# Kernel tuning notes

Hardware: AMD Instinct MI355X
Metric: run time of the kernel (lower is better)

## Reference

```python
import jax, jax.numpy as jnp
import numpy as np

B, T, D, HS = 4, 2048, 1024, 64


def setup_inputs() -> dict:
    key = jax.random.key(0)
    ks = jax.random.split(key, 8)
    s = 0.02
    return {
        "x": jax.random.normal(ks[0], (B, T, D), dtype=jnp.float32),
        "wq": jax.random.normal(ks[1], (D, HS), dtype=jnp.float32) * s,
        "bq": jax.random.normal(ks[2], (HS,), dtype=jnp.float32) * s,
        "wk": jax.random.normal(ks[3], (D, HS), dtype=jnp.float32) * s,
        "bk": jax.random.normal(ks[4], (HS,), dtype=jnp.float32) * s,
        "wv": jax.random.normal(ks[5], (D, HS), dtype=jnp.float32) * s,
        "bv": jax.random.normal(ks[6], (HS,), dtype=jnp.float32) * s,
        "rel_pos_embd": jax.random.normal(ks[7], (T, T, HS), dtype=jnp.float32) * s,
    }


def reference(x, wq, bq, wk, bk, wv, bv, rel_pos_embd):
    # x: [B,T,D]
    q = jnp.einsum("btd,dh->bth", x, wq) + bq  # [B,T,HS]
    k = jnp.einsum("btd,dh->bth", x, wk) + bk
    v = jnp.einsum("btd,dh->bth", x, wv) + bv
    hs = k.shape[-1]
    # faithful to torch: scores = QK^T / hs**(-0.5) == QK^T * sqrt(hs)
    scores = jnp.einsum("bth,bvh->btv", q, k) * jnp.sqrt(jnp.float32(hs))
    # relative-position bias (mask=False branch)
    rel = jnp.einsum("btc,tvc->btv", q, rel_pos_embd[:q.shape[1], :q.shape[1]])
    att = jax.nn.softmax(scores + rel, axis=-1)  # [B,T,T]
    return jnp.einsum("btv,bvh->bth", att, v)  # [B,T,HS]
```

## Files before the change

kernel.cpp:

```cpp
#include <hip/hip_runtime.h>

#define B_ 4
#define T_ 2048
#define D_ 1024
#define HS_ 64

typedef __attribute__((ext_vector_type(4))) float f32x4;
typedef __attribute__((ext_vector_type(8))) short bf16x8;
typedef __attribute__((ext_vector_type(4))) unsigned short u16x4;
typedef __attribute__((ext_vector_type(4))) unsigned int u32x4;

__device__ __forceinline__ unsigned short f2bf(float f) {
  unsigned int u = __float_as_uint(f);
  u += 0x7FFFu + ((u >> 16) & 1u);
  return (unsigned short)(u >> 16);
}

__global__ void kconv_kernel(const float* __restrict__ wq, const float* __restrict__ wk,
                             const float* __restrict__ wv,
                             unsigned short* __restrict__ wTh, unsigned short* __restrict__ wTl) {
  int gid = blockIdx.x * 256 + threadIdx.x;
  int n = gid >> 10, d = gid & 1023;
  float v;
  if (n < 64)        v = wq[d * 64 + n];
  else if (n < 128)  v = 8.0f * wk[d * 64 + (n - 64)];
  else               v = wv[d * 64 + (n - 128)];
  unsigned short h = f2bf(v);
  wTh[gid] = h;
  wTl[gid] = f2bf(v - __uint_as_float(((unsigned int)h) << 16));
}

__global__ __launch_bounds__(256) void kproj_kernel(
    const float* __restrict__ x, const unsigned short* __restrict__ wTh,
    const unsigned short* __restrict__ wTl,
    const float* __restrict__ bq, const float* __restrict__ bk, const float* __restrict__ bv,
    float* __restrict__ qw, float* __restrict__ k8w, unsigned short* __restrict__ vtw) {
  __shared__ unsigned short xh[32 * 32], xl[32 * 32];
  __shared__ unsigned short wh[192 * 32], wl[192 * 32];
  const int tid = threadIdx.x;
  const int m0 = blockIdx.x * 32;
  const int lane = tid & 63, wid = tid >> 6;
  const int mf = wid & 1, np = wid >> 1;
  const int r15 = lane & 15, u = lane >> 4;

  f32x4 xv;
  f32x4 wvh[3], wvl[3];
  auto issue = [&](int k0) {
    xv = *(const f32x4*)&x[(m0 + (tid >> 3)) * 1024 + k0 + (tid & 7) * 4];
#pragma unroll
    for (int i = 0; i < 3; ++i) {
      int c8 = i * 256 + tid;
      wvh[i] = *(const f32x4*)&wTh[(c8 >> 2) * 1024 + k0 + (c8 & 3) * 8];
      wvl[i] = *(const f32x4*)&wTl[(c8 >> 2) * 1024 + k0 + (c8 & 3) * 8];
    }
  };
  auto commit = [&]() {
    u16x4 hhv, llv;
#pragma unroll
    for (int c = 0; c < 4; ++c) {
      unsigned short h = f2bf(xv[c]);
      hhv[c] = h;
      llv[c] = f2bf(xv[c] - __uint_as_float(((unsigned int)h) << 16));
    }
    *(u16x4*)&xh[(tid >> 3) * 32 + (tid & 7) * 4] = hhv;
    *(u16x4*)&xl[(tid >> 3) * 32 + (tid & 7) * 4] = llv;
#pragma unroll
    for (int i = 0; i < 3; ++i) {
      int c8 = i * 256 + tid;
      *(f32x4*)&wh[c8 * 8] = wvh[i];
      *(f32x4*)&wl[c8 * 8] = wvl[i];
    }
  };

  f32x4 z = {0.f, 0.f, 0.f, 0.f};
  f32x4 acc[6] = {z, z, z, z, z, z};
  issue(0);
  for (int kt = 0; kt < 32; ++kt) {
    __syncthreads();
    commit();
    __syncthreads();
    if (kt + 1 < 32) issue((kt + 1) * 32);
    bf16x8 ah = *(const bf16x8*)&xh[(mf * 16 + r15) * 32 + u * 8];
    bf16x8 al = *(const bf16x8*)&xl[(mf * 16 + r15) * 32 + u * 8];
#pragma unroll
    for (int nf = 0; nf < 6; ++nf) {
      int nr = np * 96 + nf * 16 + r15;
      bf16x8 bh = *(const bf16x8*)&wh[nr * 32 + u * 8];
      bf16x8 bl = *(const bf16x8*)&wl[nr * 32 + u * 8];
      acc[nf] = __builtin_amdgcn_mfma_f32_16x16x32_bf16(ah, bh, acc[nf], 0, 0, 0);
      acc[nf] = __builtin_amdgcn_mfma_f32_16x16x32_bf16(ah, bl, acc[nf], 0, 0, 0);
      acc[nf] = __builtin_amdgcn_mfma_f32_16x16x32_bf16(al, bh, acc[nf], 0, 0, 0);
    }
  }
#pragma unroll
  for (int nf = 0; nf < 6; ++nf) {
    const int n = np * 96 + nf * 16 + r15;
#pragma unroll
    for (int r = 0; r < 4; ++r) {
      const int m = m0 + mf * 16 + u * 4 + r;
      float val = acc[nf][r];
      if (n < 64) {
        qw[m * 64 + n] = val + bq[n];
      } else if (n < 128) {
        k8w[m * 64 + (n - 64)] = val + 8.0f * bk[n - 64];
      } else {
        int h = n - 128;
        int bb = m >> 11, t = m & 2047;
        vtw[(bb * 64 + h) * 2048 + t] = f2bf(val + bv[h]);
      }
    }
  }
}

__global__ __launch_bounds__(256, 2) void k1_scores(
    const float* __restrict__ qw, const float* __restrict__ k8w,
    const float* __restrict__ rel, float* __restrict__ S) {
  __shared__ float rl[2][64 * 68];
  __shared__ float kl[2][32 * 68];
  const int tid = threadIdx.x;
  const int tt = blockIdx.x >> 1, vh = blockIdx.x & 1;
  const int t0 = tt * 8;
  const int vbase = vh * 1024;
  const int wid = tid >> 6;
  const int tl = (tid >> 5) & 1;
  const int vl = (tid >> 2) & 7;
  const int hq = tid & 3;
  const int tloc = wid * 2 + tl;
  const int tg = t0 + tloc;

  f32x4 qr[4][4];
#pragma unroll
  for (int b = 0; b < 4; ++b)
#pragma unroll
    for (int j = 0; j < 4; ++j)
      qr[b][j] = *(const f32x4*)&qw[((b << 11) + tg) * 64 + hq * 16 + j * 4];

  f32x4 st[6];
  auto issue = [&](int vt) {
#pragma unroll
    for (int i = 0; i < 4; ++i) {
      int c4 = i * 256 + tid;
      int pr = c4 >> 4, c = c4 & 15;
      st[i] = *(const f32x4*)&rel[(t0 + (pr >> 3)) * 131072 + (vt + (pr & 7)) * 64 + c * 4];
    }
#pragma unroll
    for (int i = 0; i < 2; ++i) {
      int c4 = i * 256 + tid;
      int pr = c4 >> 4, c = c4 & 15;
      st[4 + i] = *(const f32x4*)&k8w[(pr >> 3) * 131072 + (vt + (pr & 7)) * 64 + c * 4];
    }
  };
  auto commit = [&](int buf) {
#pragma unroll
    for (int i = 0; i < 4; ++i) {
      int c4 = i * 256 + tid;
      int pr = c4 >> 4, c = c4 & 15;
      *(f32x4*)&rl[buf][pr * 68 + c * 4] = st[i];
    }
#pragma unroll
    for (int i = 0; i < 2; ++i) {
      int c4 = i * 256 + tid;
      int pr = c4 >> 4, c = c4 & 15;
      *(f32x4*)&kl[buf][pr * 68 + c * 4] = st[4 + i];
    }
  };

  issue(vbase);
  commit(0);
  __syncthreads();
  int cur = 0;
  for (int it = 0; it < 128; ++it) {
    const int vt = vbase + it * 8;
    if (it + 1 < 128) issue(vt + 8);
    f32x4 z = {0.f, 0.f, 0.f, 0.f};
    f32x4 a0 = z, a1 = z, a2 = z, a3 = z;
    const float* rrow = &rl[cur][(tloc * 8 + vl) * 68];
    const float* krow = &kl[cur][vl * 68];
#pragma unroll
    for (int j = 0; j < 4; ++j) {
      int c = (hq * 4 + j) * 4;
      f32x4 r4 = *(const f32x4*)&rrow[c];
      f32x4 kb0 = *(const f32x4*)&krow[c];
      f32x4 kb1 = *(const f32x4*)&krow[544 + c];
      f32x4 kb2 = *(const f32x4*)&krow[1088 + c];
      f32x4 kb3 = *(const f32x4*)&krow[1632 + c];
      a0 += qr[0][j] * (kb0 + r4);
      a1 += qr[1][j] * (kb1 + r4);
      a2 += qr[2][j] * (kb2 + r4);
      a3 += qr[3][j] * (kb3 + r4);
    }
    float s0 = a0[0] + a0[1] + a0[2] + a0[3];
    float s1 = a1[0] + a1[1] + a1[2] + a1[3];
    float s2 = a2[0] + a2[1] + a2[2] + a2[3];
    float s3 = a3[0] + a3[1] + a3[2] + a3[3];
    s0 += __shfl_xor(s0, 1); s0 += __shfl_xor(s0, 2);
    s1 += __shfl_xor(s1, 1); s1 += __shfl_xor(s1, 2);
    s2 += __shfl_xor(s2, 1); s2 += __shfl_xor(s2, 2);
    s3 += __shfl_xor(s3, 1); s3 += __shfl_xor(s3, 2);
    float out = (hq == 0) ? s0 : (hq == 1) ? s1 : (hq == 2) ? s2 : s3;
    S[hq * 4194304 + tg * 2048 + vt + vl] = out;
    __syncthreads();
    if (it + 1 < 128) commit(cur ^ 1);
    __syncthreads();
    cur ^= 1;
  }
}

__global__ __launch_bounds__(256) void k2_softpv(
    const float* __restrict__ S, const unsigned short* __restrict__ vtw,
    float* __restrict__ O) {
  __shared__ float sl[2][32 * 68];
  __shared__ unsigned short vtl[2][64 * 72];
  __shared__ unsigned short ps[32 * 80];
  __shared__ float mrun[32], lrun[32], asc[32];
  const int tid = threadIdx.x;
  const int b = blockIdx.x >> 6, tt = blockIdx.x & 63;
  const int t0 = tt * 32;
  const int lane = tid & 63, wid = tid >> 6;
  const int mf = wid & 1, np = wid >> 1;
  const int r15 = lane & 15, u = lane >> 4;
  const int row = tid >> 3, vg = tid & 7;

  if (tid < 32) { mrun[tid] = -3.0e38f; lrun[tid] = 0.0f; }

  f32x4 stS[2], stV[2];
  auto issue = [&](int v0) {
#pragma unroll
    for (int i = 0; i < 2; ++i) {
      int c4 = i * 256 + tid;
      int pr = c4 >> 4, c = c4 & 15;
      stS[i] = *(const f32x4*)&S[b * 4194304 + (t0 + pr) * 2048 + v0 + c * 4];
    }
#pragma unroll
    for (int i = 0; i < 2; ++i) {
      int c8 = i * 256 + tid;
      int hr = c8 >> 3, cc = c8 & 7;
      stV[i] = *(const f32x4*)&vtw[(b * 64 + hr) * 2048 + v0 + cc * 8];
    }
  };
  auto commit = [&](int buf) {
#pragma unroll
    for (int i = 0; i < 2; ++i) {
      int c4 = i * 256 + tid;
      int pr = c4 >> 4, c = c4 & 15;
      *(f32x4*)&sl[buf][pr * 68 + c * 4] = stS[i];
    }
#pragma unroll
    for (int i = 0; i < 2; ++i) {
      int c8 = i * 256 + tid;
      int hr = c8 >> 3, cc = c8 & 7;
      *(f32x4*)&vtl[buf][hr * 72 + cc * 8] = stV[i];
    }
  };

  issue(0);
  commit(0);
  __syncthreads();

  f32x4 accA = {0.f, 0.f, 0.f, 0.f}, accB = accA;
  int cur = 0;
  for (int it = 0; it < 32; ++it) {
    if (it + 1 < 32) issue((it + 1) * 64);
    f32x4 sa = *(const f32x4*)&sl[cur][row * 68 + vg * 8];
    f32x4 sb = *(const f32x4*)&sl[cur][row * 68 + vg * 8 + 4];
    float mx = fmaxf(fmaxf(fmaxf(sa[0], sa[1]), fmaxf(sa[2], sa[3])),
                     fmaxf(fmaxf(sb[0], sb[1]), fmaxf(sb[2], sb[3])));
    mx = fmaxf(mx, __shfl_xor(mx, 1));
    mx = fmaxf(mx, __shfl_xor(mx, 2));
    mx = fmaxf(mx, __shfl_xor(mx, 4));
    float mold = mrun[row];
    float mnew = fmaxf(mold, mx);
    float alpha = __expf(mold - mnew);
    f32x4 pa, pb;
#pragma unroll
    for (int c = 0; c < 4; ++c) {
      pa[c] = __expf(sa[c] - mnew);
      pb[c] = __expf(sb[c] - mnew);
    }
    float psum = pa[0] + pa[1] + pa[2] + pa[3] + pb[0] + pb[1] + pb[2] + pb[3];
    psum += __shfl_xor(psum, 1);
    psum += __shfl_xor(psum, 2);
    psum += __shfl_xor(psum, 4);
    if (vg == 0) {
      mrun[row] = mnew;
      lrun[row] = alpha * lrun[row] + psum;
      asc[row] = alpha;
    }
    u32x4 pw;
    pw[0] = (unsigned int)f2bf(pa[0]) | ((unsigned int)f2bf(pa[1]) << 16);
    pw[1] = (unsigned int)f2bf(pa[2]) | ((unsigned int)f2bf(pa[3]) << 16);
    pw[2] = (unsigned int)f2bf(pb[0]) | ((unsigned int)f2bf(pb[1]) << 16);
    pw[3] = (unsigned int)f2bf(pb[2]) | ((unsigned int)f2bf(pb[3]) << 16);
    *(u32x4*)&ps[row * 80 + vg * 8] = pw;
    __syncthreads();
    float al0 = asc[mf * 16 + u * 4 + 0];
    float al1 = asc[mf * 16 + u * 4 + 1];
    float al2 = asc[mf * 16 + u * 4 + 2];
    float al3 = asc[mf * 16 + u * 4 + 3];
    accA[0] *= al0; accA[1] *= al1; accA[2] *= al2; accA[3] *= al3;
    accB[0] *= al0; accB[1] *= al1; accB[2] *= al2; accB[3] *= al3;
#pragma unroll
    for (int ks = 0; ks < 2; ++ks) {
      bf16x8 af = *(const bf16x8*)&ps[(mf * 16 + r15) * 80 + ks * 32 + u * 8];
      bf16x8 b0 = *(const bf16x8*)&vtl[cur][(np * 32 + r15) * 72 + ks * 32 + u * 8];
      bf16x8 b1 = *(const bf16x8*)&vtl[cur][(np * 32 + 16 + r15) * 72 + ks * 32 + u * 8];
      accA = __builtin_amdgcn_mfma_f32_16x16x32_bf16(af, b0, accA, 0, 0, 0);
      accB = __builtin_amdgcn_mfma_f32_16x16x32_bf16(af, b1, accB, 0, 0, 0);
    }
    if (it + 1 < 32) commit(cur ^ 1);
    __syncthreads();
    cur ^= 1;
  }
#pragma unroll
  for (int r = 0; r < 4; ++r) {
    float linv = 1.0f / lrun[mf * 16 + u * 4 + r];
    int trow = t0 + mf * 16 + u * 4 + r;
    O[((b << 11) + trow) * 64 + np * 32 + r15] = accA[r] * linv;
    O[((b << 11) + trow) * 64 + np * 32 + 16 + r15] = accB[r] * linv;
  }
}

extern "C" void kernel_launch(void* const* d_in, const int* in_sizes, int n_in,
                              void* d_out, int out_size, void* d_ws, size_t ws_size,
                              hipStream_t stream) {
  const float* x   = (const float*)d_in[0];
  const float* wq  = (const float*)d_in[1];
  const float* bq  = (const float*)d_in[2];
  const float* wk  = (const float*)d_in[3];
  const float* bk  = (const float*)d_in[4];
  const float* wv  = (const float*)d_in[5];
  const float* bv  = (const float*)d_in[6];
  const float* rel = (const float*)d_in[7];
  float* O = (float*)d_out;

  char* ws = (char*)d_ws;
  float* S             = (float*)(ws);
  float* qw            = (float*)(ws + 67108864);
  float* k8w           = (float*)(ws + 69206016);
  unsigned short* vtw  = (unsigned short*)(ws + 71303168);
  unsigned short* wTh  = (unsigned short*)(ws + 72351744);
  unsigned short* wTl  = (unsigned short*)(ws + 72744960);

  kconv_kernel<<<dim3(768), dim3(256), 0, stream>>>(wq, wk, wv, wTh, wTl);
  kproj_kernel<<<dim3(256), dim3(256), 0, stream>>>(x, wTh, wTl, bq, bk, bv, qw, k8w, vtw);
  k1_scores<<<dim3(512), dim3(256), 0, stream>>>(qw, k8w, rel, S);
  k2_softpv<<<dim3(256), dim3(256), 0, stream>>>(S, vtw, O);
}
```

Measured before the change: 353.9 us.

## Fuse score computation with online softmax and PV, add split-combine kernel

Merges the score kernel and the softmax-PV kernel into one: each thread keeps running max/sum and a 64-float output accumulator, reading bf16 V rows from shared memory staged alongside rel and K. This removes the 64MB fp32 score buffer write and read-back. The two v-halves produce partial outputs plus (m, l), which a small combine kernel merges. In exchange it uses scalar FMAs instead of MFMA for PV, holds 64 accumulator registers per thread, and adds a cross-lane output reduction.

```diff
diff --git a/kernel.cpp b/kernel.cpp
--- a/kernel.cpp
+++ b/kernel.cpp
@@ -14,6 +14,9 @@
   unsigned int u = __float_as_uint(f);
   u += 0x7FFFu + ((u >> 16) & 1u);
   return (unsigned short)(u >> 16);
+}
+__device__ __forceinline__ float bf2f(unsigned short s) {
+  return __uint_as_float(((unsigned int)s) << 16);
 }
 
 __global__ void kconv_kernel(const float* __restrict__ wq, const float* __restrict__ wk,
@@ -34,7 +37,7 @@
     const float* __restrict__ x, const unsigned short* __restrict__ wTh,
     const unsigned short* __restrict__ wTl,
     const float* __restrict__ bq, const float* __restrict__ bk, const float* __restrict__ bv,
-    float* __restrict__ qw, float* __restrict__ k8w, unsigned short* __restrict__ vtw) {
+    float* __restrict__ qw, float* __restrict__ k8w, unsigned short* __restrict__ vbw) {
   __shared__ unsigned short xh[32 * 32], xl[32 * 32];
   __shared__ unsigned short wh[192 * 32], wl[192 * 32];
   const int tid = threadIdx.x;
@@ -105,18 +108,19 @@
         k8w[m * 64 + (n - 64)] = val + 8.0f * bk[n - 64];
       } else {
         int h = n - 128;
-        int bb = m >> 11, t = m & 2047;
-        vtw[(bb * 64 + h) * 2048 + t] = f2bf(val + bv[h]);
+        vbw[m * 64 + h] = f2bf(val + bv[h]);
       }
     }
   }
 }
 
-__global__ __launch_bounds__(256, 2) void k1_scores(
+__global__ __launch_bounds__(256, 2) void kfused(
     const float* __restrict__ qw, const float* __restrict__ k8w,
-    const float* __restrict__ rel, float* __restrict__ S) {
+    const unsigned short* __restrict__ vbw, const float* __restrict__ rel,
+    float* __restrict__ Oh, float* __restrict__ ml2) {
   __shared__ float rl[2][64 * 68];
   __shared__ float kl[2][32 * 68];
+  __shared__ unsigned short vt_[2][32 * 76];
   const int tid = threadIdx.x;
   const int tt = blockIdx.x >> 1, vh = blockIdx.x & 1;
   const int t0 = tt * 8;
@@ -136,6 +140,7 @@
       qr[b][j] = *(const f32x4*)&qw[((b << 11) + tg) * 64 + hq * 16 + j * 4];
 
   f32x4 st[6];
+  f32x4 vstg;
   auto issue = [&](int vt) {
 #pragma unroll
     for (int i = 0; i < 4; ++i) {
@@ -149,6 +154,10 @@
       int pr = c4 >> 4, c = c4 & 15;
       st[4 + i] = *(const f32x4*)&k8w[(pr >> 3) * 131072 + (vt + (pr & 7)) * 64 + c * 4];
     }
+    {
+      int pr = tid >> 3, cc = tid & 7;
+      vstg = *(const f32x4*)&vbw[(((pr >> 3) << 11) + vt + (pr & 7)) * 64 + cc * 8];
+    }
   };
   auto commit = [&](int buf) {
 #pragma unroll
@@ -163,7 +172,18 @@
       int pr = c4 >> 4, c = c4 & 15;
       *(f32x4*)&kl[buf][pr * 68 + c * 4] = st[4 + i];
     }
+    {
+      int pr = tid >> 3, cc = tid & 7;
+      const u16x4* pv = (const u16x4*)&vstg;
+      *(u16x4*)&vt_[buf][pr * 76 + cc * 8] = pv[0];
+      *(u16x4*)&vt_[buf][pr * 76 + cc * 8 + 4] = pv[1];
+    }
   };
+
+  float o[64];
+#pragma unroll
+  for (int h = 0; h < 64; ++h) o[h] = 0.0f;
+  float mrun = -3.0e38f, lrun = 0.0f;
 
   issue(vbase);
   commit(0);
@@ -197,127 +217,67 @@
     s1 += __shfl_xor(s1, 1); s1 += __shfl_xor(s1, 2);
     s2 += __shfl_xor(s2, 1); s2 += __shfl_xor(s2, 2);
     s3 += __shfl_xor(s3, 1); s3 += __shfl_xor(s3, 2);
-    float out = (hq == 0) ? s0 : (hq == 1) ? s1 : (hq == 2) ? s2 : s3;
-    S[hq * 4194304 + tg * 2048 + vt + vl] = out;
+    float s = (hq == 0) ? s0 : (hq == 1) ? s1 : (hq == 2) ? s2 : s3;
+    float mx = s;
+    mx = fmaxf(mx, __shfl_xor(mx, 4));
+    mx = fmaxf(mx, __shfl_xor(mx, 8));
+    mx = fmaxf(mx, __shfl_xor(mx, 16));
+    float mnew = fmaxf(mrun, mx);
+    float alpha = __expf(mrun - mnew);
+    float p = __expf(s - mnew);
+    float ps_ = p;
+    ps_ += __shfl_xor(ps_, 4);
+    ps_ += __shfl_xor(ps_, 8);
+    ps_ += __shfl_xor(ps_, 16);
+    lrun = alpha * lrun + ps_;
+    mrun = mnew;
+#pragma unroll
+    for (int h = 0; h < 64; ++h) o[h] *= alpha;
+    const unsigned short* vrow = &vt_[cur][(hq * 8 + vl) * 76];
+#pragma unroll
+    for (int k = 0; k < 16; ++k) {
+      u16x4 vv = *(const u16x4*)&vrow[k * 4];
+#pragma unroll
+      for (int j = 0; j < 4; ++j)
+        o[k * 4 + j] = fmaf(p, bf2f(vv[j]), o[k * 4 + j]);
+    }
     __syncthreads();
     if (it + 1 < 128) commit(cur ^ 1);
     __syncthreads();
     cur ^= 1;
   }
-}
-
-__global__ __launch_bounds__(256) void k2_softpv(
-    const float* __restrict__ S, const unsigned short* __restrict__ vtw,
+#pragma unroll
+  for (int h = 0; h < 64; ++h) {
+    o[h] += __shfl_xor(o[h], 4);
+    o[h] += __shfl_xor(o[h], 8);
+    o[h] += __shfl_xor(o[h], 16);
+  }
+  const int orow = (vh * 4 + hq) * 2048 + tg;
+#pragma unroll
+  for (int j = 0; j < 8; ++j)
+    Oh[orow * 64 + vl * 8 + j] = o[vl * 8 + j];
+  if (vl == 0) {
+    ml2[orow * 2] = mrun;
+    ml2[orow * 2 + 1] = lrun;
+  }
+}
+
+__global__ __launch_bounds__(256) void kcomb(
+    const float* __restrict__ Oh, const float* __restrict__ ml2,
     float* __restrict__ O) {
-  __shared__ float sl[2][32 * 68];
-  __shared__ unsigned short vtl[2][64 * 72];
-  __shared__ unsigned short ps[32 * 80];
-  __shared__ float mrun[32], lrun[32], asc[32];
-  const int tid = threadIdx.x;
-  const int b = blockIdx.x >> 6, tt = blockIdx.x & 63;
-  const int t0 = tt * 32;
-  const int lane = tid & 63, wid = tid >> 6;
-  const int mf = wid & 1, np = wid >> 1;
-  const int r15 = lane & 15, u = lane >> 4;
-  const int row = tid >> 3, vg = tid & 7;
-
-  if (tid < 32) { mrun[tid] = -3.0e38f; lrun[tid] = 0.0f; }
-
-  f32x4 stS[2], stV[2];
-  auto issue = [&](int v0) {
-#pragma unroll
-    for (int i = 0; i < 2; ++i) {
-      int c4 = i * 256 + tid;
-      int pr = c4 >> 4, c = c4 & 15;
-      stS[i] = *(const f32x4*)&S[b * 4194304 + (t0 + pr) * 2048 + v0 + c * 4];
-    }
-#pragma unroll
-    for (int i = 0; i < 2; ++i) {
-      int c8 = i * 256 + tid;
-      int hr = c8 >> 3, cc = c8 & 7;
-      stV[i] = *(const f32x4*)&vtw[(b * 64 + hr) * 2048 + v0 + cc * 8];
-    }
-  };
-  auto commit = [&](int buf) {
-#pragma unroll
-    for (int i = 0; i < 2; ++i) {
-      int c4 = i * 256 + tid;
-      int pr = c4 >> 4, c = c4 & 15;
-      *(f32x4*)&sl[buf][pr * 68 + c * 4] = stS[i];
-    }
-#pragma unroll
-    for (int i = 0; i < 2; ++i) {
-      int c8 = i * 256 + tid;
-      int hr = c8 >> 3, cc = c8 & 7;
-      *(f32x4*)&vtl[buf][hr * 72 + cc * 8] = stV[i];
-    }
-  };
-
-  issue(0);
-  commit(0);
-  __syncthreads();
-
-  f32x4 accA = {0.f, 0.f, 0.f, 0.f}, accB = accA;
-  int cur = 0;
-  for (int it = 0; it < 32; ++it) {
-    if (it + 1 < 32) issue((it + 1) * 64);
-    f32x4 sa = *(const f32x4*)&sl[cur][row * 68 + vg * 8];
-    f32x4 sb = *(const f32x4*)&sl[cur][row * 68 + vg * 8 + 4];
-    float mx = fmaxf(fmaxf(fmaxf(sa[0], sa[1]), fmaxf(sa[2], sa[3])),
-                     fmaxf(fmaxf(sb[0], sb[1]), fmaxf(sb[2], sb[3])));
-    mx = fmaxf(mx, __shfl_xor(mx, 1));
-    mx = fmaxf(mx, __shfl_xor(mx, 2));
-    mx = fmaxf(mx, __shfl_xor(mx, 4));
-    float mold = mrun[row];
-    float mnew = fmaxf(mold, mx);
-    float alpha = __expf(mold - mnew);
-    f32x4 pa, pb;
-#pragma unroll
-    for (int c = 0; c < 4; ++c) {
-      pa[c] = __expf(sa[c] - mnew);
-      pb[c] = __expf(sb[c] - mnew);
-    }
-    float psum = pa[0] + pa[1] + pa[2] + pa[3] + pb[0] + pb[1] + pb[2] + pb[3];
-    psum += __shfl_xor(psum, 1);
-    psum += __shfl_xor(psum, 2);
-    psum += __shfl_xor(psum, 4);
-    if (vg == 0) {
-      mrun[row] = mnew;
-      lrun[row] = alpha * lrun[row] + psum;
-      asc[row] = alpha;
-    }
-    u32x4 pw;
-    pw[0] = (unsigned int)f2bf(pa[0]) | ((unsigned int)f2bf(pa[1]) << 16);
-    pw[1] = (unsigned int)f2bf(pa[2]) | ((unsigned int)f2bf(pa[3]) << 16);
-    pw[2] = (unsigned int)f2bf(pb[0]) | ((unsigned int)f2bf(pb[1]) << 16);
-    pw[3] = (unsigned int)f2bf(pb[2]) | ((unsigned int)f2bf(pb[3]) << 16);
-    *(u32x4*)&ps[row * 80 + vg * 8] = pw;
-    __syncthreads();
-    float al0 = asc[mf * 16 + u * 4 + 0];
-    float al1 = asc[mf * 16 + u * 4 + 1];
-    float al2 = asc[mf * 16 + u * 4 + 2];
-    float al3 = asc[mf * 16 + u * 4 + 3];
-    accA[0] *= al0; accA[1] *= al1; accA[2] *= al2; accA[3] *= al3;
-    accB[0] *= al0; accB[1] *= al1; accB[2] *= al2; accB[3] *= al3;
-#pragma unroll
-    for (int ks = 0; ks < 2; ++ks) {
-      bf16x8 af = *(const bf16x8*)&ps[(mf * 16 + r15) * 80 + ks * 32 + u * 8];
-      bf16x8 b0 = *(const bf16x8*)&vtl[cur][(np * 32 + r15) * 72 + ks * 32 + u * 8];
-      bf16x8 b1 = *(const bf16x8*)&vtl[cur][(np * 32 + 16 + r15) * 72 + ks * 32 + u * 8];
-      accA = __builtin_amdgcn_mfma_f32_16x16x32_bf16(af, b0, accA, 0, 0, 0);
-      accB = __builtin_amdgcn_mfma_f32_16x16x32_bf16(af, b1, accB, 0, 0, 0);
-    }
-    if (it + 1 < 32) commit(cur ^ 1);
-    __syncthreads();
-    cur ^= 1;
-  }
-#pragma unroll
-  for (int r = 0; r < 4; ++r) {
-    float linv = 1.0f / lrun[mf * 16 + u * 4 + r];
-    int trow = t0 + mf * 16 + u * 4 + r;
-    O[((b << 11) + trow) * 64 + np * 32 + r15] = accA[r] * linv;
-    O[((b << 11) + trow) * 64 + np * 32 + 16 + r15] = accB[r] * linv;
-  }
+  int gid = blockIdx.x * 256 + threadIdx.x;
+  int row = gid >> 4, hc = gid & 15;
+  float m0 = ml2[row * 2], l0 = ml2[row * 2 + 1];
+  float m1 = ml2[(8192 + row) * 2], l1 = ml2[(8192 + row) * 2 + 1];
+  float m = fmaxf(m0, m1);
+  float c0 = __expf(m0 - m), c1 = __expf(m1 - m);
+  float linv = 1.0f / (c0 * l0 + c1 * l1);
+  f32x4 o0 = *(const f32x4*)&Oh[row * 64 + hc * 4];
+  f32x4 o1 = *(const f32x4*)&Oh[(8192 + row) * 64 + hc * 4];
+  f32x4 r;
+#pragma unroll
+  for (int j = 0; j < 4; ++j) r[j] = (c0 * o0[j] + c1 * o1[j]) * linv;
+  *(f32x4*)&O[row * 64 + hc * 4] = r;
 }
 
 extern "C" void kernel_launch(void* const* d_in, const int* in_sizes, int n_in,
@@ -334,15 +294,16 @@
   float* O = (float*)d_out;
 
   char* ws = (char*)d_ws;
-  float* S             = (float*)(ws);
-  float* qw            = (float*)(ws + 67108864);
-  float* k8w           = (float*)(ws + 69206016);
-  unsigned short* vtw  = (unsigned short*)(ws + 71303168);
-  unsigned short* wTh  = (unsigned short*)(ws + 72351744);
-  unsigned short* wTl  = (unsigned short*)(ws + 72744960);
+  float* qw            = (float*)(ws);
+  float* k8w           = (float*)(ws + 2097152);
+  unsigned short* vbw  = (unsigned short*)(ws + 4194304);
+  unsigned short* wTh  = (unsigned short*)(ws + 5242880);
+  unsigned short* wTl  = (unsigned short*)(ws + 5636096);
+  float* Oh            = (float*)(ws + 6291456);
+  float* ml2           = (float*)(ws + 10485760);
 
   kconv_kernel<<<dim3(768), dim3(256), 0, stream>>>(wq, wk, wv, wTh, wTl);
-  kproj_kernel<<<dim3(256), dim3(256), 0, stream>>>(x, wTh, wTl, bq, bk, bv, qw, k8w, vtw);
-  k1_scores<<<dim3(512), dim3(256), 0, stream>>>(qw, k8w, rel, S);
-  k2_softpv<<<dim3(256), dim3(256), 0, stream>>>(S, vtw, O);
-}
+  kproj_kernel<<<dim3(256), dim3(256), 0, stream>>>(x, wTh, wTl, bq, bk, bv, qw, k8w, vbw);
+  kfused<<<dim3(512), dim3(256), 0, stream>>>(qw, k8w, vbw, rel, Oh, ml2);
+  kcomb<<<dim3(512), dim3(256), 0, stream>>>(Oh, ml2, O);
+}
```

Measured after the change: 831.6 us. 2.35x slower.
